# Kernel optimization log

Measured on AMD Instinct MI355X. Metric: run time of the kernel, lower is better.

Reference implementation:

```python
import jax, jax.numpy as jnp
import numpy as np

R = 4           # max_displacement
P = 2 * R + 1   # search_range = 9
DILATIONS = [[1], [1, 2, 3, 5, 9, 16]]
STRIDES = [4, 1]  # 8 // encoder_output_stride for strides [2, 8]
EPS = 1e-9


def _l2norm(x):
    # torch: x / (x.norm(dim=1, keepdim=True) + 1e-9)
    return x / (jnp.linalg.norm(x, axis=1, keepdims=True) + EPS)


def _corr(x1, x2, dilation, stride):
    """SpatialCorrelationSampler(patch_size=9, stride=stride, padding=0,
    dilation_patch=dilation): out[b,u,v,i,j] = sum_c x1[b,c,i*s,j*s] *
    x2[b,c,i*s+(u-R)*d, j*s+(v-R)*d], zero outside bounds."""
    B, C, H, W = x1.shape
    pad = R * dilation
    x2p = jnp.pad(x2, ((0, 0), (0, 0), (pad, pad), (pad, pad)))
    x1s = x1[:, :, ::stride, ::stride]  # (B,C,Ho,Wo)
    Ho, Wo = x1s.shape[2], x1s.shape[3]
    # all 81 (u,v) patch-offset slice starts in the padded map
    uv = jnp.stack(jnp.meshgrid(jnp.arange(P), jnp.arange(P), indexing='ij'),
                   axis=-1).reshape(-1, 2) * dilation  # (81, 2)

    def step(carry, start):
        x2uv = jax.lax.dynamic_slice(x2p, (0, 0, start[0], start[1]), (B, C, H, W))
        x2uv = x2uv[:, :, ::stride, ::stride]
        return carry, jnp.sum(x1s * x2uv, axis=1)  # (B,Ho,Wo)

    _, cost = jax.lax.scan(step, None, uv)  # (81,B,Ho,Wo)
    cost = cost.reshape(P, P, B, Ho, Wo)
    return jnp.transpose(cost, (2, 0, 1, 3, 4))  # (B,P,P,Ho,Wo)


def setup_inputs() -> dict:
    key = jax.random.key(0)
    k0, k1, k2, k3 = jax.random.split(key, 4)
    return {
        'x1_0': jax.random.normal(k0, (4, 256, 192, 256), dtype=jnp.float32),
        'x1_1': jax.random.normal(k1, (4, 256, 48, 64), dtype=jnp.float32),
        'x2_0': jax.random.normal(k2, (4, 256, 192, 256), dtype=jnp.float32),
        'x2_1': jax.random.normal(k3, (4, 256, 48, 64), dtype=jnp.float32),
    }


def reference(x1_0, x1_1, x2_0, x2_1):
    xs1, xs2 = [x1_0, x1_1], [x2_0, x2_1]
    cost_list = []
    for x1, x2, dils, s in zip(xs1, xs2, DILATIONS, STRIDES):
        x1n = _l2norm(x1)
        x2n = _l2norm(x2)
        per_dil = [_corr(x1n, x2n, d, s) for d in dils]  # each (B,P,P,Ho,Wo)
        # num_groups=1: per-dilation volumes stack into dim 1
        cost_list.append(jnp.stack(per_dil, axis=1))  # (B,nd,P,P,Ho,Wo)
    return jnp.concatenate(cost_list, axis=1)  # (B,7,9,9,48,64)
```

## Files before the change

### kernel.cpp

```cpp
#include <hip/hip_runtime.h>
#include <stdint.h>

#define EPSN 1e-9f

typedef __fp16 f16x8 __attribute__((ext_vector_type(8)));
typedef float f32x4 __attribute__((ext_vector_type(4)));

#define LDS_FENCE()                                        \
  do {                                                     \
    asm volatile("s_waitcnt lgkmcnt(0)" ::: "memory");     \
    __builtin_amdgcn_sched_barrier(0);                     \
  } while (0)


__global__ __launch_bounds__(256) void norms1_kernel(
    const float* __restrict__ x1_1, const float* __restrict__ x2_1,
    float* __restrict__ ws) {
  int p = blockIdx.x * 256 + threadIdx.x;
  const float* src = (p < 12288) ? x1_1 : x2_1;
  int q = (p < 12288) ? p : p - 12288;
  long base = (long)(q / 3072) * 786432 + (q % 3072);
  float ss = 0.f;
#pragma unroll 8
  for (int c = 0; c < 256; ++c) { float v = src[base + (long)c * 3072]; ss += v * v; }
  ws[p] = 1.f / (sqrtf(ss) + EPSN);
}

__global__ __launch_bounds__(256) void corr0_kernel(
    const float* __restrict__ x1, const float* __restrict__ x2,
    float* __restrict__ out) {
  int bx = blockIdx.x;
  int L = (bx & 7) * 96 + (bx >> 3);
  int y = L % 192, b = L / 192;
  int tid = threadIdx.x;
  int w = tid >> 6, lane = tid & 63;
  int i_lo = (y - 1) / 4; if (i_lo < 0) i_lo = 0;
  int i_hi = (y + 4) / 4; if (i_hi > 47) i_hi = 47;
  int NI = i_hi - i_lo + 1;

  __shared__ float red[4][34][64];
  __shared__ float inv2s[264];
  __shared__ float inv1s[3][64];

  float acc[3][9];
#pragma unroll
  for (int r = 0; r < 3; ++r)
#pragma unroll
    for (int v = 0; v < 9; ++v) acc[r][v] = 0.f;
  float sq0 = 0.f, sq1 = 0.f, sq2 = 0.f, sq3 = 0.f;
  float s1[3] = {0.f, 0.f, 0.f};

  const float* x2mid = x2 + (long)b * 12582912 + (long)y * 256 + 4 * lane;
  const float* x2lo  = x2mid - ((lane == 0) ? 0 : 4);
  const float* x2hi  = x2mid + ((lane == 63) ? 3 : 4);
  const float* x1p[3];
#pragma unroll
  for (int r = 0; r < 3; ++r) {
    int ir = i_lo + r; if (ir > 47) ir = 47;
    x1p[r] = x1 + (long)b * 12582912 + (long)(4 * ir) * 256 + 4 * lane;
  }

#pragma unroll 8
  for (int cc = 0; cc < 64; ++cc) {
    long off = (long)(w * 64 + cc) * 49152;
    float4 fm = *reinterpret_cast<const float4*>(x2mid + off);
    float4 fl = *reinterpret_cast<const float4*>(x2lo + off);
    float fh = x2hi[off];
    sq0 += fm.x * fm.x; sq1 += fm.y * fm.y; sq2 += fm.z * fm.z; sq3 += fm.w * fm.w;
#pragma unroll
    for (int r = 0; r < 3; ++r) {
      float xv = x1p[r][off];
      s1[r] += xv * xv;
      acc[r][0] += xv * fl.x; acc[r][1] += xv * fl.y;
      acc[r][2] += xv * fl.z; acc[r][3] += xv * fl.w;
      acc[r][4] += xv * fm.x; acc[r][5] += xv * fm.y;
      acc[r][6] += xv * fm.z; acc[r][7] += xv * fm.w;
      acc[r][8] += xv * fh;
    }
  }

#pragma unroll
  for (int r = 0; r < 3; ++r) {
#pragma unroll
    for (int v = 0; v < 9; ++v) red[w][r * 9 + v][lane] = acc[r][v];
    red[w][31 + r][lane] = s1[r];
  }
  red[w][27][lane] = sq0; red[w][28][lane] = sq1;
  red[w][29][lane] = sq2; red[w][30][lane] = sq3;
  __syncthreads();
  {
    int comp = tid & 3, jj = tid >> 2;
    float ss = red[0][27 + comp][jj] + red[1][27 + comp][jj] +
               red[2][27 + comp][jj] + red[3][27 + comp][jj];
    inv2s[4 + tid] = 1.f / (sqrtf(ss) + EPSN);
    if (tid < 4) { inv2s[tid] = 0.f; inv2s[260 + tid] = 0.f; }
    if (tid < 192) {
      int r = tid >> 6, j = tid & 63;
      float t = red[0][31 + r][j] + red[1][31 + r][j] +
                red[2][31 + r][j] + red[3][31 + r][j];
      inv1s[r][j] = 1.f / (sqrtf(t) + EPSN);
    }
  }
  __syncthreads();
  int lim = NI * 576;
  for (int idx = tid; idx < lim; idx += 256) {
    int r = idx / 576, rem = idx - r * 576;
    int v = rem >> 6, j = rem & 63;
    int i_r = i_lo + r;
    int u_r = y - 4 * i_r + 4;
    float s = red[0][r * 9 + v][j] + red[1][r * 9 + v][j] +
              red[2][r * 9 + v][j] + red[3][r * 9 + v][j];
    out[(long)b * 1741824 + (long)u_r * 27648 + (long)v * 3072 + i_r * 64 + j] =
        s * inv1s[r][j] * inv2s[4 * j + v];
  }
}

__global__ __launch_bounds__(256) void zfill0_kernel(float* __restrict__ out) {
  int idx = blockIdx.x * 256 + threadIdx.x;
  int b = idx / 2880, rem = idx - b * 2880;
  int k = rem / 576, rem2 = rem - k * 576;
  int v = rem2 >> 6, j = rem2 & 63;
  int u = (k < 4) ? k : 8;
  int i = (k < 4) ? 0 : 47;
  out[(long)b * 1741824 + (long)u * 27648 + (long)v * 3072 + i * 64 + j] = 0.f;
}

__global__ __launch_bounds__(256) void xpose1_kernel(
    const float* __restrict__ x1, const float* __restrict__ x2,
    __fp16* __restrict__ o1, __fp16* __restrict__ o2) {
  int bx = blockIdx.x;
  int tz = bx & 1; int rem = bx >> 1;
  int i = rem % 48, b = rem / 48;
  const float* src = tz ? x2 : x1;
  __fp16* dst = (tz ? o2 : o1) + (long)(b * 48 + i) * 16384;
  __shared__ uint32_t lds[64 * 128];
  __shared__ float sred[4][64];
  int t = threadIdx.x;
  int j = t & 63, cg = t >> 6;
  const float* sp = src + (long)b * 786432 + (long)i * 64 + j;
  float ss = 0.f;
#pragma unroll 8
  for (int c8 = 0; c8 < 64; ++c8) {
    float v = sp[(long)(cg * 64 + c8) * 3072];
    ss += v * v;
  }
  sred[cg][j] = ss;
  __syncthreads();
  float invv = 1.f / (sqrtf(sred[0][j] + sred[1][j] + sred[2][j] + sred[3][j]) + EPSN);
#pragma unroll
  for (int cb = 0; cb < 8; ++cb) {
    uint32_t pk[4];
#pragma unroll
    for (int e2 = 0; e2 < 4; ++e2) {
      int c0 = cg * 64 + cb * 8 + e2 * 2;
      __fp16 h0 = (__fp16)(sp[(long)c0 * 3072] * invv);
      __fp16 h1 = (__fp16)(sp[(long)(c0 + 1) * 3072] * invv);
      pk[e2] = (uint32_t)__builtin_bit_cast(uint16_t, h0) |
               ((uint32_t)__builtin_bit_cast(uint16_t, h1) << 16);
    }
    int byteoff = j * 512 + ((cg * 128 + cb * 16) ^ ((j & 7) << 4));
    *reinterpret_cast<uint4*>(reinterpret_cast<char*>(lds) + byteoff) =
        make_uint4(pk[0], pk[1], pk[2], pk[3]);
  }
  __syncthreads();
#pragma unroll
  for (int rep = 0; rep < 8; ++rep) {
    int idx = rep * 256 + t;
    int jj = idx >> 5, cb = idx & 31;
    int byteoff = jj * 512 + ((cb * 16) ^ ((jj & 7) << 4));
    uint4 val = *reinterpret_cast<const uint4*>(
        reinterpret_cast<const char*>(lds) + byteoff);
    *reinterpret_cast<uint4*>(reinterpret_cast<char*>(dst) + jj * 512 + cb * 16) = val;
  }
}

__device__ const int OFFS39[39] = {
    0, 1, -1, 2, -2, 3, -3, 4, -4, 5, -5, 6, -6, 8, -8, 9, -9, 10, -10,
    12, -12, 15, -15, 16, -16, 18, -18, 20, -20, 27, -27, 32, -32, 36, -36,
    48, -48, 64, -64};

__global__ __launch_bounds__(64) void corr1m_kernel(
    const __fp16* __restrict__ w1, const __fp16* __restrict__ w2,
    float* __restrict__ out) {
  const int dils[6] = {1, 2, 3, 5, 9, 16};
  int bx = blockIdx.x;
  int L = (bx & 7) * 936 + (bx >> 3);
  int oi = L % 39, i = (L / 39) % 48, b = L / 1872;
  int o = OFFS39[oi];
  int y = i + o;
  bool valid = (y >= 0 && y < 48);
  int l = threadIdx.x;
  __shared__ float c_lds[64][65];

  if (valid) {
    int lm = l & 15, lk = l >> 4;
    const __fp16* A = w1 + (long)(b * 48 + i) * 16384;
    const __fp16* B = w2 + (long)(b * 48 + y) * 16384;
    f32x4 acc[4][4];
#pragma unroll
    for (int tm = 0; tm < 4; ++tm)
#pragma unroll
      for (int tn = 0; tn < 4; ++tn) acc[tm][tn] = (f32x4)0.f;

    for (int ks = 0; ks < 8; ++ks) {
      f16x8 af[4], bf[4];
      int ko = ks * 32 + lk * 8;
#pragma unroll
      for (int tm = 0; tm < 4; ++tm)
        af[tm] = __builtin_bit_cast(f16x8, *reinterpret_cast<const uint4*>(
                     A + (tm * 16 + lm) * 256 + ko));
#pragma unroll
      for (int tn = 0; tn < 4; ++tn)
        bf[tn] = __builtin_bit_cast(f16x8, *reinterpret_cast<const uint4*>(
                     B + (tn * 16 + lm) * 256 + ko));
#pragma unroll
      for (int tm = 0; tm < 4; ++tm)
#pragma unroll
        for (int tn = 0; tn < 4; ++tn)
          acc[tm][tn] = __builtin_amdgcn_mfma_f32_16x16x32_f16(
              af[tm], bf[tn], acc[tm][tn], 0, 0, 0);
    }
#pragma unroll
    for (int tm = 0; tm < 4; ++tm)
#pragma unroll
      for (int tn = 0; tn < 4; ++tn)
#pragma unroll
        for (int r = 0; r < 4; ++r)
          c_lds[tm * 16 + lk * 4 + r][tn * 16 + lm] = acc[tm][tn][r];
    LDS_FENCE();
  }

#pragma unroll
  for (int dI = 0; dI < 6; ++dI) {
    int d = dils[dI];
    if (o % d) continue;
    int ud = o / d;
    if (ud < -4 || ud > 4) continue;
    long ob = (long)b * 1741824 + (long)(1 + dI) * 248832 +
              (long)(ud + 4) * 27648 + (long)i * 64 + l;
#pragma unroll
    for (int v = 0; v < 9; ++v) {
      float val = 0.f;
      if (valid) {
        int j2 = l + (v - 4) * d;
        val = (j2 >= 0 && j2 < 64) ? c_lds[l][j2] : 0.f;
      }
      out[ob + (long)v * 3072] = val;
    }
  }
}

__global__ __launch_bounds__(64) void corr1_kernel(
    const float* __restrict__ x1, const float* __restrict__ x2,
    const float* __restrict__ ws, float* __restrict__ out) {
  int bx = blockIdx.x;
  int L = (bx & 7) * 1296 + (bx >> 3);
  int u = L % 9, dI = (L / 9) % 6, i = (L / 54) % 48, b = L / 2592;
  const int dils[6] = {1, 2, 3, 5, 9, 16};
  int d = dils[dI];
  int y = i + (u - 4) * d;
  int lane = threadIdx.x;
  long ob = (long)b * 1741824 + (long)(1 + dI) * 248832 + (long)u * 27648 +
            (long)i * 64 + lane;
  if (y < 0 || y >= 48) {
#pragma unroll
    for (int v = 0; v < 9; ++v) out[ob + v * 3072] = 0.f;
    return;
  }
  __shared__ uint4 x2t[192];
  x2t[lane] = make_uint4(0, 0, 0, 0);
  x2t[lane + 64] = make_uint4(0, 0, 0, 0);
  x2t[lane + 128] = make_uint4(0, 0, 0, 0);
  float acc[9];
#pragma unroll
  for (int v = 0; v < 9; ++v) acc[v] = 0.f;
  const float* x2row = x2 + (long)b * 786432 + (long)y * 64 + lane;
  const float* x1row = x1 + (long)b * 786432 + (long)i * 64 + lane;
#pragma unroll 1
  for (int cc8 = 0; cc8 < 32; ++cc8) {
    float x1v[8]; uint32_t xb[8];
#pragma unroll
    for (int cc = 0; cc < 8; ++cc) {
      long c = cc8 * 8 + cc;
      xb[cc] = __float_as_uint(x2row[c * 3072]) + 0x8000u;
      x1v[cc] = x1row[c * 3072];
    }
    uint4 pk;
    pk.x = (xb[0] >> 16) | (xb[1] & 0xffff0000u);
    pk.y = (xb[2] >> 16) | (xb[3] & 0xffff0000u);
    pk.z = (xb[4] >> 16) | (xb[5] & 0xffff0000u);
    pk.w = (xb[6] >> 16) | (xb[7] & 0xffff0000u);
    x2t[64 + lane] = pk;
    LDS_FENCE();
#pragma unroll
    for (int v = 0; v < 9; ++v) {
      uint4 q = x2t[64 + lane + (v - 4) * d];
      float s;
      s  = x1v[0] * __uint_as_float(q.x << 16);
      s += x1v[1] * __uint_as_float(q.x & 0xffff0000u);
      s += x1v[2] * __uint_as_float(q.y << 16);
      s += x1v[3] * __uint_as_float(q.y & 0xffff0000u);
      s += x1v[4] * __uint_as_float(q.z << 16);
      s += x1v[5] * __uint_as_float(q.z & 0xffff0000u);
      s += x1v[6] * __uint_as_float(q.w << 16);
      s += x1v[7] * __uint_as_float(q.w & 0xffff0000u);
      acc[v] += s;
    }
    LDS_FENCE();
  }
  const float* i1 = ws + b * 3072 + i * 64;
  const float* i2 = ws + 12288 + b * 3072 + y * 64;
  float inv1 = i1[lane];
#pragma unroll
  for (int v = 0; v < 9; ++v) {
    int col = lane + (v - 4) * d;
    float i2v = (col >= 0 && col < 64) ? i2[col] : 0.f;
    out[ob + v * 3072] = acc[v] * inv1 * i2v;
  }
}

extern "C" void kernel_launch(void* const* d_in, const int* in_sizes, int n_in,
                              void* d_out, int out_size, void* d_ws, size_t ws_size,
                              hipStream_t stream) {
  const float* x1_0 = (const float*)d_in[0];
  const float* x1_1 = (const float*)d_in[1];
  const float* x2_0 = (const float*)d_in[2];
  const float* x2_1 = (const float*)d_in[3];
  float* out = (float*)d_out;
  float* ws = (float*)d_ws;
  corr0_kernel<<<768, 256, 0, stream>>>(x1_0, x2_0, out);
  zfill0_kernel<<<45, 256, 0, stream>>>(out);
  if (ws_size >= 12681216) {
    __fp16* w1h = (__fp16*)((char*)d_ws + 98304);
    __fp16* w2h = w1h + 3145728;
    xpose1_kernel<<<384, 256, 0, stream>>>(x1_1, x2_1, w1h, w2h);
    corr1m_kernel<<<7488, 64, 0, stream>>>(w1h, w2h, out);
  } else {
    norms1_kernel<<<96, 256, 0, stream>>>(x1_1, x2_1, ws);
    corr1_kernel<<<10368, 64, 0, stream>>>(x1_1, x2_1, ws, out);
  }
}
```

Before: 140.4 us.

## Split corr0 channel reduction across 8 waves with chunked LDS reduction

Raises corr0_kernel from 256 to 512 threads, so each of 8 waves reduces 32 channels instead of 64. To keep the LDS footprint small, the cross-wave reduction buffer shrinks to 14 rows and is reused: norms are reduced first, then the 27 accumulators are written and summed in two passes. The aim is more waves in flight to hide the latency of the streaming loads. The cost is extra barriers, a longer cross-wave reduction, and a lower unroll factor.

```diff
diff --git a/kernel.cpp b/kernel.cpp
--- a/kernel.cpp
+++ b/kernel.cpp
@@ -26,7 +26,7 @@
   ws[p] = 1.f / (sqrtf(ss) + EPSN);
 }
 
-__global__ __launch_bounds__(256) void corr0_kernel(
+__global__ __launch_bounds__(512, 4) void corr0_kernel(
     const float* __restrict__ x1, const float* __restrict__ x2,
     float* __restrict__ out) {
   int bx = blockIdx.x;
@@ -38,7 +38,7 @@
   int i_hi = (y + 4) / 4; if (i_hi > 47) i_hi = 47;
   int NI = i_hi - i_lo + 1;
 
-  __shared__ float red[4][34][64];
+  __shared__ float red[8][14][64];
   __shared__ float inv2s[264];
   __shared__ float inv1s[3][64];
 
@@ -53,65 +53,103 @@
   const float* x2mid = x2 + (long)b * 12582912 + (long)y * 256 + 4 * lane;
   const float* x2lo  = x2mid - ((lane == 0) ? 0 : 4);
   const float* x2hi  = x2mid + ((lane == 63) ? 3 : 4);
-  const float* x1p[3];
-#pragma unroll
-  for (int r = 0; r < 3; ++r) {
-    int ir = i_lo + r; if (ir > 47) ir = 47;
-    x1p[r] = x1 + (long)b * 12582912 + (long)(4 * ir) * 256 + 4 * lane;
-  }
-
-#pragma unroll 8
-  for (int cc = 0; cc < 64; ++cc) {
-    long off = (long)(w * 64 + cc) * 49152;
+  const float* x1p0, *x1p1, *x1p2;
+  {
+    int i1c = i_lo + 1, i2c = i_lo + 2;
+    if (i1c > 47) i1c = 47;
+    if (i2c > 47) i2c = 47;
+    x1p0 = x1 + (long)b * 12582912 + (long)(4 * i_lo) * 256 + 4 * lane;
+    x1p1 = x1 + (long)b * 12582912 + (long)(4 * i1c) * 256 + 4 * lane;
+    x1p2 = x1 + (long)b * 12582912 + (long)(4 * i2c) * 256 + 4 * lane;
+  }
+
+#pragma unroll 2
+  for (int cc = 0; cc < 32; ++cc) {
+    long off = (long)(w * 32 + cc) * 49152;
     float4 fm = *reinterpret_cast<const float4*>(x2mid + off);
     float4 fl = *reinterpret_cast<const float4*>(x2lo + off);
     float fh = x2hi[off];
+    float xa = x1p0[off], xb = x1p1[off], xc = x1p2[off];
     sq0 += fm.x * fm.x; sq1 += fm.y * fm.y; sq2 += fm.z * fm.z; sq3 += fm.w * fm.w;
-#pragma unroll
-    for (int r = 0; r < 3; ++r) {
-      float xv = x1p[r][off];
-      s1[r] += xv * xv;
-      acc[r][0] += xv * fl.x; acc[r][1] += xv * fl.y;
-      acc[r][2] += xv * fl.z; acc[r][3] += xv * fl.w;
-      acc[r][4] += xv * fm.x; acc[r][5] += xv * fm.y;
-      acc[r][6] += xv * fm.z; acc[r][7] += xv * fm.w;
-      acc[r][8] += xv * fh;
-    }
-  }
-
-#pragma unroll
-  for (int r = 0; r < 3; ++r) {
-#pragma unroll
-    for (int v = 0; v < 9; ++v) red[w][r * 9 + v][lane] = acc[r][v];
-    red[w][31 + r][lane] = s1[r];
-  }
-  red[w][27][lane] = sq0; red[w][28][lane] = sq1;
-  red[w][29][lane] = sq2; red[w][30][lane] = sq3;
-  __syncthreads();
-  {
+    s1[0] += xa * xa;
+    acc[0][0] += xa * fl.x; acc[0][1] += xa * fl.y;
+    acc[0][2] += xa * fl.z; acc[0][3] += xa * fl.w;
+    acc[0][4] += xa * fm.x; acc[0][5] += xa * fm.y;
+    acc[0][6] += xa * fm.z; acc[0][7] += xa * fm.w;
+    acc[0][8] += xa * fh;
+    s1[1] += xb * xb;
+    acc[1][0] += xb * fl.x; acc[1][1] += xb * fl.y;
+    acc[1][2] += xb * fl.z; acc[1][3] += xb * fl.w;
+    acc[1][4] += xb * fm.x; acc[1][5] += xb * fm.y;
+    acc[1][6] += xb * fm.z; acc[1][7] += xb * fm.w;
+    acc[1][8] += xb * fh;
+    s1[2] += xc * xc;
+    acc[2][0] += xc * fl.x; acc[2][1] += xc * fl.y;
+    acc[2][2] += xc * fl.z; acc[2][3] += xc * fl.w;
+    acc[2][4] += xc * fm.x; acc[2][5] += xc * fm.y;
+    acc[2][6] += xc * fm.z; acc[2][7] += xc * fm.w;
+    acc[2][8] += xc * fh;
+  }
+
+  red[w][0][lane] = sq0; red[w][1][lane] = sq1;
+  red[w][2][lane] = sq2; red[w][3][lane] = sq3;
+  red[w][4][lane] = s1[0]; red[w][5][lane] = s1[1]; red[w][6][lane] = s1[2];
+  __syncthreads();
+  if (tid < 256) {
     int comp = tid & 3, jj = tid >> 2;
-    float ss = red[0][27 + comp][jj] + red[1][27 + comp][jj] +
-               red[2][27 + comp][jj] + red[3][27 + comp][jj];
+    float ss = 0.f;
+#pragma unroll
+    for (int ww = 0; ww < 8; ++ww) ss += red[ww][comp][jj];
     inv2s[4 + tid] = 1.f / (sqrtf(ss) + EPSN);
-    if (tid < 4) { inv2s[tid] = 0.f; inv2s[260 + tid] = 0.f; }
-    if (tid < 192) {
-      int r = tid >> 6, j = tid & 63;
-      float t = red[0][31 + r][j] + red[1][31 + r][j] +
-                red[2][31 + r][j] + red[3][31 + r][j];
-      inv1s[r][j] = 1.f / (sqrtf(t) + EPSN);
-    }
-  }
-  __syncthreads();
-  int lim = NI * 576;
-  for (int idx = tid; idx < lim; idx += 256) {
-    int r = idx / 576, rem = idx - r * 576;
-    int v = rem >> 6, j = rem & 63;
-    int i_r = i_lo + r;
-    int u_r = y - 4 * i_r + 4;
-    float s = red[0][r * 9 + v][j] + red[1][r * 9 + v][j] +
-              red[2][r * 9 + v][j] + red[3][r * 9 + v][j];
-    out[(long)b * 1741824 + (long)u_r * 27648 + (long)v * 3072 + i_r * 64 + j] =
-        s * inv1s[r][j] * inv2s[4 * j + v];
+  } else if (tid < 264) {
+    int e = tid - 256;
+    inv2s[(e < 4) ? e : (256 + e)] = 0.f;
+  } else if (tid >= 320) {
+    int r = (tid - 320) >> 6, j = tid & 63;
+    float t = 0.f;
+#pragma unroll
+    for (int ww = 0; ww < 8; ++ww) t += red[ww][4 + r][j];
+    inv1s[r][j] = 1.f / (sqrtf(t) + EPSN);
+  }
+  __syncthreads();
+
+#pragma unroll
+  for (int ar = 0; ar < 14; ++ar) {
+    int r = (ar >= 9) ? 1 : 0, v = ar - r * 9;
+    red[w][ar][lane] = acc[r][v];
+  }
+  __syncthreads();
+  for (int idx = tid; idx < 14 * 64; idx += 512) {
+    int ar = idx >> 6, j = idx & 63;
+    int r = (ar >= 9) ? 1 : 0, v = ar - r * 9;
+    if (r < NI) {
+      float s = 0.f;
+#pragma unroll
+      for (int ww = 0; ww < 8; ++ww) s += red[ww][ar][j];
+      int i_r = i_lo + r, u_r = y - 4 * i_r + 4;
+      out[(long)b * 1741824 + (long)u_r * 27648 + (long)v * 3072 + i_r * 64 + j] =
+          s * inv1s[r][j] * inv2s[4 * j + v];
+    }
+  }
+  __syncthreads();
+
+#pragma unroll
+  for (int ar = 14; ar < 27; ++ar) {
+    int r = (ar >= 18) ? 2 : 1, v = ar - r * 9;
+    red[w][ar - 14][lane] = acc[r][v];
+  }
+  __syncthreads();
+  for (int idx = tid; idx < 13 * 64; idx += 512) {
+    int ar = 14 + (idx >> 6), j = idx & 63;
+    int r = (ar >= 18) ? 2 : 1, v = ar - r * 9;
+    if (r < NI) {
+      float s = 0.f;
+#pragma unroll
+      for (int ww = 0; ww < 8; ++ww) s += red[ww][ar - 14][j];
+      int i_r = i_lo + r, u_r = y - 4 * i_r + 4;
+      out[(long)b * 1741824 + (long)u_r * 27648 + (long)v * 3072 + i_r * 64 + j] =
+          s * inv1s[r][j] * inv2s[4 * j + v];
+    }
   }
 }
 
@@ -328,7 +366,7 @@
   const float* x2_1 = (const float*)d_in[3];
   float* out = (float*)d_out;
   float* ws = (float*)d_ws;
-  corr0_kernel<<<768, 256, 0, stream>>>(x1_0, x2_0, out);
+  corr0_kernel<<<768, 512, 0, stream>>>(x1_0, x2_0, out);
   zfill0_kernel<<<45, 256, 0, stream>>>(out);
   if (ws_size >= 12681216) {
     __fp16* w1h = (__fp16*)((char*)d_ws + 98304);
```

Measured after the change: 133.5 us. -4.9%, faster.
